# Performance work log

Measured on AMD Instinct MI355X. Metric: run time of the kernel, lower is better.

The kernel has to match this reference:

```python
import jax, jax.numpy as jnp
import numpy as np

B, N, D = 16, 512, 768
HEADS = 3
NEG_INF = -1e9


def _lin(k, o, i):
    s = 1.0 / np.sqrt(i)
    return jax.random.uniform(k, (o, i), jnp.float32, -s, s)


def setup_inputs() -> dict:
    key = jax.random.key(0)
    ks = jax.random.split(key, 20)
    adj = jax.random.uniform(ks[0], (B, N, N), jnp.float32)
    inputs = jax.random.normal(ks[1], (B, N, D), jnp.float32)
    # padding-style mask: last quarter of key positions masked (True = masked)
    score_mask = jnp.broadcast_to((jnp.arange(N) >= (3 * N) // 4)[None, None, None, :], (B, HEADS, N, N))
    Dh = 2 * D  # concat dim at layer 1
    return {
        'adj': adj,
        'inputs': inputs,
        'score_mask': score_mask,
        'W0_w': _lin(ks[2], D, D), 'W0_b': jnp.zeros((D,), jnp.float32),
        'W1_w': _lin(ks[3], D, Dh), 'W1_b': jnp.zeros((D,), jnp.float32),
        'conv_w': jax.random.normal(ks[4], (N, N, 3), jnp.float32) * (1.0 / np.sqrt(3 * N)),
        'conv_b': jnp.zeros((N,), jnp.float32),
        'linearc_w': _lin(ks[5], D, D - 2), 'linearc_b': jnp.zeros((D,), jnp.float32),
        'fc1_w': _lin(ks[6], D, D), 'fc2_w': _lin(ks[7], D, D),
        'attn_q_w': _lin(ks[8], Dh, Dh), 'attn_q_b': jnp.zeros((Dh,), jnp.float32),
        'attn_k_w': _lin(ks[9], Dh, Dh), 'attn_k_b': jnp.zeros((Dh,), jnp.float32),
    }


def _gcn_layer(adj, x, denom, Ww, Wb):
    Ax = jnp.einsum('bij,bjd->bid', adj, x)          # adj.bmm(x)
    AxW = (Ax @ Ww.T + Wb) / denom
    return jax.nn.relu(AxW) + (x @ Ww.T + Wb)


def reference(adj, inputs, score_mask, W0_w, W0_b, W1_w, W1_b, conv_w, conv_b,
              linearc_w, linearc_b, fc1_w, fc2_w, attn_q_w, attn_q_b, attn_k_w, attn_k_b):
    denom = adj.sum(2, keepdims=True) + 1.0
    out = _gcn_layer(adj, inputs, denom, W0_w, W0_b)            # [B,N,768]
    # Conv1d(n, n, 3): tokens as channels, features as length -> [B,N,766]
    conve = jax.lax.conv_general_dilated(out, conv_w, (1,), 'VALID',
                                         dimension_numbers=('NCH', 'OIH', 'NCH'))
    conve = jax.nn.relu(conve + conv_b[None, :, None])
    out = conve @ linearc_w.T + linearc_b                       # [B,N,768]

    x = jnp.concatenate([inputs, out], axis=-1)                 # [B,N,1536]
    Dh = x.shape[-1]
    d_k = Dh // HEADS
    q = (x @ attn_q_w.T + attn_q_b).reshape(B, N, HEADS, d_k).transpose(0, 2, 1, 3)
    k = (x @ attn_k_w.T + attn_k_b).reshape(B, N, HEADS, d_k).transpose(0, 2, 1, 3)
    scores = jnp.einsum('bhqd,bhkd->bhqk', q, k) / jnp.sqrt(jnp.float32(d_k))
    scores = jnp.where(score_mask, NEG_INF, scores)
    bmask = (~score_mask[:, :, :, 0:1]).astype(scores.dtype)    # [B,H,N,1]
    p_attn = jax.nn.softmax(scores, axis=-1) * bmask            # [B,H,N,N]

    sums = p_attn.sum(axis=(-2, -1))                            # [B,H]
    prob = jax.nn.softmax(sums, axis=0)                         # softmax over batch dim, as in source
    max_idx = jnp.argmax(prob, axis=1)                          # [B]
    adj2 = jnp.take_along_axis(p_attn, max_idx[:, None, None, None], axis=1)[:, 0]  # [B,N,N]

    # select(adj2, 2) * adj2 -- source mutates adj in place, so the RHS adj is binarized too
    flat = adj2.reshape(B, -1)
    thr = jax.lax.top_k(flat, 2)[0][:, 1]                       # 2nd-largest per batch
    bbin = (flat >= thr[:, None]).astype(adj2.dtype).reshape(B, N, N)
    M = bbin + jnp.swapaxes(bbin, -1, -2)
    eye = jnp.eye(N, dtype=adj2.dtype)
    M = M * (1.0 - eye) + eye                                   # fill_diagonal_(1)
    adj2 = M * bbin

    denom2 = adj2.sum(2, keepdims=True) + 1.0
    out = _gcn_layer(adj2, x, denom2, W1_w, W1_b)               # [B,N,768]
    out = jax.nn.relu(out @ fc1_w.T) @ fc2_w.T                  # fc (no biases)
    return out
```

## Files before the change

### kernel.cpp

```cpp
#include <hip/hip_runtime.h>
#include <math.h>


namespace {

constexpr long long O_DEN  = 0;
constexpr long long O_DEN2 = 8192;
constexpr long long O_SUMP = 16384;
constexpr long long O_THR  = 17920;
constexpr long long O_MIDX = 17936;
constexpr long long O_CNT  = 17952;
constexpr long long O_POS  = 17968;
constexpr long long O_T2P  = 18224;
constexpr long long O_NNZC = 19456;
constexpr long long O_NNZJ = 27648;
constexpr long long O_NNZV = 60416;
constexpr long long O_QKB  = 93184;

constexpr long long O_X    = 131072;
constexpr long long OZ     = 131072 + 12582912;
constexpr long long TOTAL_FLOATS = OZ + 17825792;

typedef short bf16x8 __attribute__((ext_vector_type(8)));
typedef float f32x4 __attribute__((ext_vector_type(4)));
typedef float f32x16 __attribute__((ext_vector_type(16)));

__global__ void sentinel_kernel(float* out) {
    if (threadIdx.x == 0 && blockIdx.x == 0) out[0] = 1.0e6f;
}

__device__ __forceinline__ unsigned short bf16rne(float f) {
    union { float x; unsigned u; } a; a.x = f;
    return (unsigned short)((a.u + 0x7FFFu + ((a.u >> 16) & 1u)) >> 16);
}

__device__ __forceinline__ void cvt_split(float f, unsigned short& h, unsigned short& l) {
    union { float x; unsigned u; } a; a.x = f;
    unsigned hb = (a.u + 0x7FFFu + ((a.u >> 16) & 1u)) & 0xFFFF0000u;
    h = (unsigned short)(hb >> 16);
    union { unsigned u; float x; } b; b.u = hb;
    float r = f - b.x;
    union { float x; unsigned u; } c; c.x = r;
    l = (unsigned short)((c.u + 0x7FFFu + ((c.u >> 16) & 1u)) >> 16);
}

__device__ __forceinline__ void gl_lds16(const unsigned short* g, unsigned short* l) {
    __builtin_amdgcn_global_load_lds(
        (const __attribute__((address_space(1))) unsigned int*)g,
        (__attribute__((address_space(3))) unsigned int*)l,
        16, 0, 0);
}

__global__ void convert_planes_kernel(const float* __restrict__ src, unsigned short* __restrict__ dst,
                                      long long loOff, long long n4) {
    long long idx = (long long)blockIdx.x * 256 + threadIdx.x;
    if (idx >= n4) return;
    float4 v = ((const float4*)src)[idx];
    unsigned short h0,h1,h2,h3,l0,l1,l2,l3;
    cvt_split(v.x,h0,l0); cvt_split(v.y,h1,l1); cvt_split(v.z,h2,l2); cvt_split(v.w,h3,l3);
    uint2 hp, lp;
    hp.x = (unsigned)h0 | ((unsigned)h1 << 16); hp.y = (unsigned)h2 | ((unsigned)h3 << 16);
    lp.x = (unsigned)l0 | ((unsigned)l1 << 16); lp.y = (unsigned)l2 | ((unsigned)l3 << 16);
    *(uint2*)&dst[idx * 4] = hp;
    *(uint2*)&dst[loOff + idx * 4] = lp;
}

__global__ void convert_bf16_kernel(const float* __restrict__ src, unsigned short* __restrict__ dst,
                                    long long n4) {
    long long idx = (long long)blockIdx.x * 256 + threadIdx.x;
    if (idx >= n4) return;
    float4 v = ((const float4*)src)[idx];
    ushort4 o;
    o.x = bf16rne(v.x); o.y = bf16rne(v.y); o.z = bf16rne(v.z); o.w = bf16rne(v.w);
    *(ushort4*)&dst[idx * 4] = o;
}

__global__ void transpose_bf16_kernel(const float* __restrict__ inp, unsigned short* __restrict__ dst) {
    __shared__ float T[64][65];
    const int z = blockIdx.z;
    const int i0 = blockIdx.x * 64, d0 = blockIdx.y * 64;
    const float* src = inp + (long long)z * 393216;
    unsigned short* dz = dst + (long long)z * 393216;
    const int cl = threadIdx.x & 63, rl = threadIdx.x >> 6;
    #pragma unroll 4
    for (int e = 0; e < 16; ++e) {
        int il = e * 4 + rl;
        T[il][cl] = src[(long long)(i0 + il) * 768 + d0 + cl];
    }
    __syncthreads();
    #pragma unroll 4
    for (int e = 0; e < 16; ++e) {
        int dl = e * 4 + rl;
        dz[(long long)(d0 + dl) * 512 + i0 + cl] = bf16rne(T[cl][dl]);
    }
}

__global__ void pad_lw_kernel(const float* __restrict__ Lw, unsigned short* __restrict__ Lp) {
    int idx = blockIdx.x * 256 + threadIdx.x;
    int n = idx / 768, k = idx - n * 768;
    float v = (k < 766) ? Lw[n * 766 + k] : 0.f;
    unsigned short h, l; cvt_split(v, h, l);
    Lp[idx] = h; Lp[589824 + idx] = l;
}

__global__ void convert_qkw_kernel(const float* __restrict__ Qw, const float* __restrict__ Kw,
                                   unsigned short* __restrict__ dst) {
    long long idx = (long long)blockIdx.x * 256 + threadIdx.x;
    if (idx >= 1179648) return;
    long long e = idx * 4;
    int h = (int)(e / 1572864);
    int rem = (int)(e - (long long)h * 1572864);
    int row = rem / 1536, k = rem - row * 1536;
    const float* src = (row < 512) ? (Qw + ((long long)(h * 512 + row) * 1536 + k))
                                   : (Kw + ((long long)(h * 512 + row - 512) * 1536 + k));
    float4 v = *(const float4*)src;
    unsigned short h0,h1,h2,h3,l0,l1,l2,l3;
    cvt_split(v.x,h0,l0); cvt_split(v.y,h1,l1); cvt_split(v.z,h2,l2); cvt_split(v.w,h3,l3);
    uint2 hp, lp;
    hp.x = (unsigned)h0 | ((unsigned)h1 << 16); hp.y = (unsigned)h2 | ((unsigned)h3 << 16);
    lp.x = (unsigned)l0 | ((unsigned)l1 << 16); lp.y = (unsigned)l2 | ((unsigned)l3 << 16);
    *(uint2*)&dst[e] = hp;
    *(uint2*)&dst[4718592 + e] = lp;
}

__global__ void qkb_kernel(const float* __restrict__ Qb, const float* __restrict__ Kb,
                           float* __restrict__ qkb) {
    int i = blockIdx.x * 256 + threadIdx.x;
    if (i >= 3072) return;
    int h = i >> 10, r = i & 1023;
    qkb[i] = (r < 512) ? Qb[h * 512 + r] : Kb[h * 512 + r - 512];
}

template<int TAG, int BMODE, int CMODE, int ONEPASS>
__global__ __launch_bounds__(256, ONEPASS ? 3 : 2)
void gemm_mfma_kernel(const unsigned short* __restrict__ Au, const void* __restrict__ Bv,
                      void* __restrict__ Cv, const float* __restrict__ bias,
                      int M, int N, int K, int lda, int ldb, int ldc,
                      long long sA, long long sB, long long sC,
                      float divd, int relu, long long aLo,
                      long long bLo, long long cLo, int Nreal)
{
    __shared__ __align__(16) unsigned short AhS[2][128][32];
    __shared__ __align__(16) unsigned short BhS[2][128][32];
    __shared__ __align__(16) unsigned short AlS[ONEPASS ? 1 : 2][128][32];
    __shared__ __align__(16) unsigned short BlS[ONEPASS ? 1 : 2][128][32];

    const int gx = gridDim.x, gy = gridDim.y;
    const int nwg = gx * gy * gridDim.z;
    const int lin = blockIdx.x + gx * (blockIdx.y + gy * blockIdx.z);
    const int q8 = nwg >> 3, r8 = nwg & 7;
    const int xcd = lin & 7, sidx = lin >> 3;
    const int nl = (xcd < r8) ? xcd * (q8 + 1) + sidx : r8 * (q8 + 1) + (xcd - r8) * q8 + sidx;
    const int bx = nl % gx;
    const int t1 = nl / gx;
    const int by = t1 % gy;
    const int z  = t1 / gy;

    const int tid = threadIdx.x;
    const int m0 = by * 128, n0 = bx * 128;
    const int lane = tid & 63, wave = tid >> 6;
    const int wm = (wave & 1) * 64, wn = (wave >> 1) * 64;
    const int lk = lane >> 5, lm = lane & 31;
    const int sxor = (lm >> 1) & 3;

    const unsigned short* A = Au + z * sA;
    const float* Bf = (const float*)Bv + z * sB;
    const unsigned short* Bu = (const unsigned short*)Bv + z * sB;
    float* Cf = (float*)Cv + z * sC;
    unsigned short* Cu = (unsigned short*)Cv + z * sC;

    f32x16 acc[2][2];
    #pragma unroll
    for (int i = 0; i < 2; ++i)
        #pragma unroll
        for (int j = 0; j < 2; ++j)
            #pragma unroll
            for (int r = 0; r < 16; ++r) acc[i][j][r] = 0.f;

    auto stage = [&](int kk, int b) {
        #pragma unroll
        for (int v = 0; v < 2; ++v) {
            const int j0 = v * 256 + (wave << 6);
            const int row0 = j0 >> 2;
            const int j = j0 + lane;
            const int row = j >> 2, c = j & 3;
            const int kch = c ^ ((row >> 1) & 3);
            const long long aoff = (long long)(m0 + row) * lda + kk + kch * 8;
            gl_lds16(A + aoff, &AhS[b][row0][0]);
            if constexpr (!ONEPASS) gl_lds16(A + aLo + aoff, &AlS[b][row0][0]);
            if constexpr (BMODE == 3) {
                const long long boff = (long long)(n0 + row) * ldb + kk + kch * 8;
                gl_lds16(Bu + boff, &BhS[b][row0][0]);
                if constexpr (!ONEPASS) gl_lds16(Bu + bLo + boff, &BlS[b][row0][0]);
            }
        }
        if constexpr (BMODE == 2) {
            #pragma unroll
            for (int v = 0; v < 2; ++v) {
                const int j = v * 256 + tid;
                const int n = j >> 2, c = j & 3;
                const int kch = c ^ ((n >> 1) & 3);
                const int k8 = kk + kch * 8;
                unsigned short hh[8], ll[8];
                #pragma unroll
                for (int e = 0; e < 8; ++e) {
                    const int kg = k8 + e;
                    const int ii = kg / 3, k3 = kg - ii * 3;
                    cvt_split(Bf[(long long)ii * 768 + (n0 + n) + k3], hh[e], ll[e]);
                }
                uint4 hp, lp;
                hp.x = (unsigned)hh[0] | ((unsigned)hh[1] << 16);
                hp.y = (unsigned)hh[2] | ((unsigned)hh[3] << 16);
                hp.z = (unsigned)hh[4] | ((unsigned)hh[5] << 16);
                hp.w = (unsigned)hh[6] | ((unsigned)hh[7] << 16);
                lp.x = (unsigned)ll[0] | ((unsigned)ll[1] << 16);
                lp.y = (unsigned)ll[2] | ((unsigned)ll[3] << 16);
                lp.z = (unsigned)ll[4] | ((unsigned)ll[5] << 16);
                lp.w = (unsigned)ll[6] | ((unsigned)ll[7] << 16);
                *(uint4*)&BhS[b][n][c * 8] = hp;
                *(uint4*)&BlS[b][n][c * 8] = lp;
            }
        }
    };

    auto compute = [&](int b) {
        #pragma unroll
        for (int ks = 0; ks < 2; ++ks) {
            const int kc = ks * 2 + lk;
            const int sl = (kc ^ sxor) * 8;
            bf16x8 ah[2], bh[2];
            #pragma unroll
            for (int i = 0; i < 2; ++i) ah[i] = *(const bf16x8*)&AhS[b][wm + i * 32 + lm][sl];
            #pragma unroll
            for (int j = 0; j < 2; ++j) bh[j] = *(const bf16x8*)&BhS[b][wn + j * 32 + lm][sl];
            if constexpr (ONEPASS) {
                #pragma unroll
                for (int i = 0; i < 2; ++i)
                    #pragma unroll
                    for (int j = 0; j < 2; ++j)
                        acc[i][j] = __builtin_amdgcn_mfma_f32_32x32x16_bf16(ah[i], bh[j], acc[i][j], 0, 0, 0);
            } else {
                bf16x8 al[2], bl[2];
                #pragma unroll
                for (int i = 0; i < 2; ++i) al[i] = *(const bf16x8*)&AlS[b][wm + i * 32 + lm][sl];
                #pragma unroll
                for (int j = 0; j < 2; ++j) bl[j] = *(const bf16x8*)&BlS[b][wn + j * 32 + lm][sl];
                #pragma unroll
                for (int i = 0; i < 2; ++i)
                    #pragma unroll
                    for (int j = 0; j < 2; ++j) {
                        acc[i][j] = __builtin_amdgcn_mfma_f32_32x32x16_bf16(ah[i], bh[j], acc[i][j], 0, 0, 0);
                        acc[i][j] = __builtin_amdgcn_mfma_f32_32x32x16_bf16(ah[i], bl[j], acc[i][j], 0, 0, 0);
                        acc[i][j] = __builtin_amdgcn_mfma_f32_32x32x16_bf16(al[i], bh[j], acc[i][j], 0, 0, 0);
                    }
            }
        }
    };

    const int nt = K >> 5;
    stage(0, 0);
    for (int t = 0; t < nt; ++t) {
        if constexpr (BMODE == 2) {
            asm volatile("s_waitcnt vmcnt(0) lgkmcnt(0)" ::: "memory");
        } else {
            asm volatile("s_waitcnt vmcnt(0)" ::: "memory");
        }
        __builtin_amdgcn_sched_barrier(0);
        __builtin_amdgcn_s_barrier();
        __builtin_amdgcn_sched_barrier(0);
        if (t + 1 < nt) stage((t + 1) << 5, (t + 1) & 1);
        __builtin_amdgcn_s_setprio(1);
        compute(t & 1);
        __builtin_amdgcn_s_setprio(0);
    }
    #pragma unroll
    for (int i = 0; i < 2; ++i) {
        #pragma unroll
        for (int j = 0; j < 2; ++j) {
            #pragma unroll
            for (int reg = 0; reg < 16; ++reg) {
                const int m = m0 + wm + i * 32 + (reg & 3) + 8 * (reg >> 2) + 4 * lk;
                const int n = n0 + wn + j * 32 + lm;
                float v = acc[i][j][reg];
                if (divd != 1.f) v = v / divd;
                if (bias) v += bias[BMODE == 2 ? m : n];
                if (relu) v = fmaxf(v, 0.f);
                if (n >= Nreal) v = 0.f;
                if constexpr (CMODE == 1) {
                    unsigned short h, l; cvt_split(v, h, l);
                    Cu[(long long)m * ldc + n] = h;
                    Cu[cLo + (long long)m * ldc + n] = l;
                } else {
                    Cf[(long long)m * ldc + n] = v;
                }
            }
        }
    }
}

__global__ void rowsum_kernel(const float* __restrict__ A, float* __restrict__ out, int ncols) {
    const float* row = A + (long long)blockIdx.x * ncols;
    float s = 0.f;
    for (int j = threadIdx.x; j < ncols; j += 256) s += row[j];
    __shared__ float red[256];
    red[threadIdx.x] = s;
    __syncthreads();
    for (int st = 128; st > 0; st >>= 1) {
        if (threadIdx.x < st) red[threadIdx.x] += red[threadIdx.x + st];
        __syncthreads();
    }
    if (threadIdx.x == 0) out[blockIdx.x] = red[0] + 1.0f;
}

__global__ void gcn_epilogue_kernel(const float* __restrict__ axw, const float* __restrict__ xw,
                                    const float* __restrict__ bias, const float* __restrict__ denom,
                                    float* __restrict__ out)
{
    long long idx = (long long)blockIdx.x * 256 + threadIdx.x;
    int m = (int)(idx / 768);
    int d = (int)(idx - (long long)m * 768);
    float bb = bias[d];
    float v = (axw[idx] + bb) / denom[m];
    out[idx] = fmaxf(v, 0.f) + xw[idx] + bb;
}

__global__ void copy_concat_kernel(const float* __restrict__ inp, unsigned short* __restrict__ xcat)
{
    long long idx = (long long)blockIdx.x * 256 + threadIdx.x;
    int m = (int)(idx / 768);
    int d = (int)(idx - (long long)m * 768);
    unsigned short h, l; cvt_split(inp[idx], h, l);
    xcat[(long long)m * 1536 + d] = h;
    xcat[12582912LL + (long long)m * 1536 + d] = l;
}

__global__ void softmax_kernel(float* __restrict__ P)
{
    float* row = P + (long long)blockIdx.x * 384;
    const int t = threadIdx.x;
    float v0 = row[t], v1 = row[t + 128], v2 = row[t + 256];
    float m = fmaxf(v0, fmaxf(v1, v2));
    #pragma unroll
    for (int off = 32; off > 0; off >>= 1) m = fmaxf(m, __shfl_down(m, off));
    __shared__ float redm[2];
    if ((t & 63) == 0) redm[t >> 6] = m;
    __syncthreads();
    m = fmaxf(redm[0], redm[1]);
    float e0 = expf(v0 - m), e1 = expf(v1 - m), e2 = expf(v2 - m);
    float s = e0 + e1 + e2;
    #pragma unroll
    for (int off = 32; off > 0; off >>= 1) s += __shfl_down(s, off);
    __shared__ float reds[2];
    if ((t & 63) == 0) reds[t >> 6] = s;
    __syncthreads();
    s = reds[0] + reds[1];
    row[t] = e0 / s;
    row[t + 128] = e1 / s;
    row[t + 256] = e2 / s;
}

__global__ void sums1_kernel(const float* __restrict__ P, double* __restrict__ sump)
{
    int blk = blockIdx.x;
    int bh = blk >> 4, ch = blk & 15;
    const float* p = P + (long long)bh * 196608 + ch * 12288;
    double s = 0.0;
    for (int i = threadIdx.x; i < 12288; i += 256) s += (double)p[i];
    __shared__ double red[256];
    red[threadIdx.x] = s;
    __syncthreads();
    for (int st = 128; st > 0; st >>= 1) {
        if (threadIdx.x < st) red[threadIdx.x] += red[threadIdx.x + st];
        __syncthreads();
    }
    if (threadIdx.x == 0) sump[blk] = red[0];
}

__global__ void decide2_kernel(const double* __restrict__ sump, int* __restrict__ maxidx)
{
    __shared__ double s48[48];
    int t = threadIdx.x;
    if (t < 48) {
        double s = 0.0;
        for (int i = 0; i < 16; ++i) s += sump[t * 16 + i];
        s48[t] = s;
    }
    __syncthreads();
    if (t == 0) {
        float s[16][3], prob[16][3];
        for (int b = 0; b < 16; ++b)
            for (int h = 0; h < 3; ++h) s[b][h] = (float)s48[b * 3 + h];
        for (int h = 0; h < 3; ++h) {
            float m = -1e30f;
            for (int b = 0; b < 16; ++b) m = fmaxf(m, s[b][h]);
            float e[16]; float Z = 0.f;
            for (int b = 0; b < 16; ++b) { e[b] = expf(s[b][h] - m); Z += e[b]; }
            for (int b = 0; b < 16; ++b) prob[b][h] = e[b] / Z;
        }
        for (int b = 0; b < 16; ++b) {
            int best = 0; float bv = prob[b][0];
            for (int h = 1; h < 3; ++h) if (prob[b][h] > bv) { bv = prob[b][h]; best = h; }
            maxidx[b] = best;
        }
    }
}

__global__ void top2a_kernel(const float* __restrict__ P, const int* __restrict__ maxidx,
                             float2* __restrict__ t2p)
{
    int blk = blockIdx.x;
    int b = blk >> 5, ch = blk & 31;
    const float* p = P + ((long long)b * 3 + maxidx[b]) * 196608 + ch * 6144;
    float m1 = -1e30f, m2 = -1e30f;
    for (int i = threadIdx.x; i < 6144; i += 256) {
        float v = p[i];
        if (v > m1) { m2 = m1; m1 = v; }
        else if (v > m2) { m2 = v; }
    }
    __shared__ float r1[256], r2[256];
    r1[threadIdx.x] = m1; r2[threadIdx.x] = m2;
    __syncthreads();
    if (threadIdx.x == 0) {
        float M1 = -1e30f, M2 = -1e30f;
        for (int i = 0; i < 256; ++i) {
            float a = r1[i], c = r2[i];
            if (a > M1) { M2 = M1; M1 = a; } else if (a > M2) { M2 = a; }
            if (c > M1) { M2 = M1; M1 = c; } else if (c > M2) { M2 = c; }
        }
        t2p[blk] = make_float2(M1, M2);
    }
}

__global__ void top2b_kernel(const float2* __restrict__ t2p, float* __restrict__ thr)
{
    int b = blockIdx.x;
    if (threadIdx.x != 0) return;
    float M1 = -1e30f, M2 = -1e30f;
    for (int i = 0; i < 32; ++i) {
        float2 v = t2p[b * 32 + i];
        if (v.x > M1) { M2 = M1; M1 = v.x; } else if (v.x > M2) { M2 = v.x; }
        if (v.y > M1) { M2 = M1; M1 = v.y; } else if (v.y > M2) { M2 = v.y; }
    }
    thr[b] = M2;
}

__global__ void init_nnz_kernel(int* __restrict__ cntb, int* __restrict__ nnzc,
                                float* __restrict__ den2)
{
    int idx = blockIdx.x * 256 + threadIdx.x;
    if (idx < 16) cntb[idx] = 0;
    if (idx < 8192) { nnzc[idx] = 0; den2[idx] = 1.f; }
}

__global__ void scan_thr_kernel(const float* __restrict__ P, const int* __restrict__ maxidx,
                                const float* __restrict__ thr, int* __restrict__ cntb,
                                int* __restrict__ pos)
{
    int blk = blockIdx.x;
    int b = blk / 12, ch = blk % 12;
    const float* p = P + ((long long)b * 3 + maxidx[b]) * 196608;
    float t = thr[b];
    int base = ch * 16384;
    for (int l = 0; l < 64; ++l) {
        int idx = base + threadIdx.x + l * 256;
        if (p[idx] >= t) {
            int q = atomicAdd(&cntb[b], 1);
            if (q < 16) {
                int i = idx / 384, j = idx - i * 384;
                pos[b * 16 + q] = (i << 16) | j;
            }
        }
    }
}

__global__ void build_nnz_kernel(const int* __restrict__ cntb, const int* __restrict__ pos,
                                 int* __restrict__ nnzc, int* __restrict__ jn,
                                 float* __restrict__ jv, float* __restrict__ den2)
{
    int b = threadIdx.x;
    if (b >= 16 || blockIdx.x != 0) return;
    int c = cntb[b]; if (c > 16) c = 16;
    for (int e = 0; e < c; ++e) {
        int pk = pos[b * 16 + e];
        int i = pk >> 16, j = pk & 0xFFFF;
        float val;
        if (i == j) val = 1.f;
        else {
            int rev = (j << 16) | i;
            int found = 0;
            for (int e2 = 0; e2 < c; ++e2) if (pos[b * 16 + e2] == rev) found = 1;
            val = 1.f + (float)found;
        }
        int r = b * 512 + i;
        int slot = nnzc[r];
        if (slot < 4) { jn[r * 4 + slot] = b * 512 + j; jv[r * 4 + slot] = val; }
        nnzc[r] = slot + 1;
        den2[r] += val;
    }
}

__global__ void gcn1_epilogue_kernel(const float* __restrict__ XW1, const float* __restrict__ b1,
                                     const float* __restrict__ den2, const int* __restrict__ cnt,
                                     const int* __restrict__ jn, const float* __restrict__ jv,
                                     unsigned short* __restrict__ outp)
{
    int m = blockIdx.x;
    int c = cnt[m]; if (c > 4) c = 4;
    float d2 = den2[m];
    int js[4]; float vs[4];
    for (int s = 0; s < c; ++s) { js[s] = jn[m * 4 + s]; vs[s] = jv[m * 4 + s]; }
    const float* xrow = XW1 + (long long)m * 768;
    #pragma unroll
    for (int l = 0; l < 3; ++l) {
        int d = threadIdx.x + l * 256;
        float ax = 0.f;
        for (int s = 0; s < c; ++s) ax += vs[s] * XW1[(long long)js[s] * 768 + d];
        float bb = b1[d];
        float v = fmaxf((ax + bb) / d2, 0.f) + xrow[d] + bb;
        unsigned short h, lo; cvt_split(v, h, lo);
        outp[(long long)m * 768 + d] = h;
        outp[6291456LL + (long long)m * 768 + d] = lo;
    }
}

}

extern "C" void kernel_launch(void* const* d_in, const int* in_sizes, int n_in,
                              void* d_out, int out_size, void* d_ws, size_t ws_size,
                              hipStream_t stream) {
    const float* adj = (const float*)d_in[0];
    const float* inp = (const float*)d_in[1];
    const float* W0w = (const float*)d_in[3];
    const float* W0b = (const float*)d_in[4];
    const float* W1w = (const float*)d_in[5];
    const float* W1b = (const float*)d_in[6];
    const float* Cw  = (const float*)d_in[7];
    const float* Cbi = (const float*)d_in[8];
    const float* Lw  = (const float*)d_in[9];
    const float* Lb  = (const float*)d_in[10];
    const float* F1  = (const float*)d_in[11];
    const float* F2  = (const float*)d_in[12];
    const float* Qw  = (const float*)d_in[13];
    const float* Qb  = (const float*)d_in[14];
    const float* Kw  = (const float*)d_in[15];
    const float* Kbi = (const float*)d_in[16];
    float* out = (float*)d_out;

    if (ws_size < (size_t)TOTAL_FLOATS * sizeof(float)) {
        sentinel_kernel<<<dim3(1), dim3(64), 0, stream>>>(out);
        return;
    }

    float* W = (float*)d_ws;
    float*   DEN   = W + O_DEN;
    float*   DEN2  = W + O_DEN2;
    double*  SUMP  = (double*)(W + O_SUMP);
    float*   THR   = W + O_THR;
    int*     MIDX  = (int*)(W + O_MIDX);
    int*     CNT   = (int*)(W + O_CNT);
    int*     POS   = (int*)(W + O_POS);
    float2*  T2P   = (float2*)(W + O_T2P);
    int*     NNZC  = (int*)(W + O_NNZC);
    int*     NNZJ  = (int*)(W + O_NNZJ);
    float*   NNZV  = W + O_NNZV;
    float*   QKB   = W + O_QKB;

    unsigned short* INPP  = (unsigned short*)(W + O_X);
    float*          OUT0  = W + O_X;
    unsigned short* XCATp = (unsigned short*)(W + O_X);
    unsigned short* F1P   = (unsigned short*)(W + O_X);
    unsigned short* F2P   = (unsigned short*)(W + O_X + 589824);

    unsigned short* AXp    = (unsigned short*)(W + OZ);
    float*          AXW0f  = W + OZ + 6291456;
    float*          XW0f   = W + O_X + 6291456;
    unsigned short* W0P    = (unsigned short*)(W + OZ + 12582912);
    unsigned short* ADJB   = (unsigned short*)(W + OZ + 13172736);
    unsigned short* CONVEp = (unsigned short*)(W + OZ);
    unsigned short* CwP    = (unsigned short*)(W + OZ + 6291456);
    unsigned short* LWPp   = (unsigned short*)(W + OZ + 7077888);
    unsigned short* QKp    = (unsigned short*)(W + OZ);
    float*          P      = W + OZ + 8388608;
    float*          XW1f   = W + OZ;
    unsigned short* OUTL1p = (unsigned short*)(W + OZ + 6291456);
    unsigned short* H1p    = (unsigned short*)(W + OZ);

    unsigned short* INPTB  = (unsigned short*)out;
    unsigned short* QKwP   = (unsigned short*)out;
    unsigned short* W1P    = (unsigned short*)(out + 4718592);

    const float divs = sqrtf(512.0f);
    const int BIGN = 1 << 30;

    convert_planes_kernel<<<dim3(6144), dim3(256), 0, stream>>>(inp, INPP, 6291456, 1572864);
    convert_planes_kernel<<<dim3(576), dim3(256), 0, stream>>>(W0w, W0P, 589824, 147456);
    convert_bf16_kernel<<<dim3(4096), dim3(256), 0, stream>>>(adj, ADJB, 1048576);
    transpose_bf16_kernel<<<dim3(8, 12, 16), dim3(256), 0, stream>>>(inp, INPTB);
    qkb_kernel<<<dim3(12), dim3(256), 0, stream>>>(Qb, Kbi, QKB);
    rowsum_kernel<<<dim3(8192), dim3(256), 0, stream>>>(adj, DEN, 512);
    gemm_mfma_kernel<0, 3, 1, 1><<<dim3(6, 4, 16), dim3(256), 0, stream>>>(
        ADJB, INPTB, AXp, nullptr, 512, 768, 512, 512, 512, 768,
        262144LL, 393216LL, 393216LL, 1.f, 0, 0, 0, 6291456LL, BIGN);
    gemm_mfma_kernel<1, 3, 0, 0><<<dim3(6, 64, 2), dim3(256), 0, stream>>>(
        INPP, W0P, XW0f, nullptr, 8192, 768, 768, 768, 768, 768,
        25165824LL, 0, 12582912LL, 1.f, 0, 6291456LL, 589824LL, 0, BIGN);
    gcn_epilogue_kernel<<<dim3(24576), dim3(256), 0, stream>>>(AXW0f, XW0f, W0b, DEN, OUT0);

    convert_planes_kernel<<<dim3(768), dim3(256), 0, stream>>>(Cw, CwP, 786432, 196608);
    pad_lw_kernel<<<dim3(2304), dim3(256), 0, stream>>>(Lw, LWPp);
    convert_qkw_kernel<<<dim3(4608), dim3(256), 0, stream>>>(Qw, Kw, QKwP);
    convert_planes_kernel<<<dim3(1152), dim3(256), 0, stream>>>(W1w, W1P, 1179648, 294912);

    gemm_mfma_kernel<2, 2, 1, 0><<<dim3(6, 4, 16), dim3(256), 0, stream>>>(
        CwP, OUT0, CONVEp, Cbi, 512, 768, 1536, 1536, 0, 768,
        0, 393216LL, 393216LL, 1.f, 1, 786432LL, 0, 6291456LL, 766);
    gemm_mfma_kernel<3, 3, 1, 0><<<dim3(6, 64, 1), dim3(256), 0, stream>>>(
        CONVEp, LWPp, (void*)(XCATp + 768), Lb, 8192, 768, 768, 768, 768, 1536,
        0, 0, 0, 1.f, 0, 6291456LL, 589824LL, 12582912LL, BIGN);
    copy_concat_kernel<<<dim3(24576), dim3(256), 0, stream>>>(inp, XCATp);

    for (int h = 0; h < 3; ++h) {
        gemm_mfma_kernel<4, 3, 1, 0><<<dim3(8, 64, 1), dim3(256), 0, stream>>>(
            XCATp, QKwP + (long long)h * 1572864, QKp, QKB + h * 1024,
            8192, 1024, 1536, 1536, 1536, 1024,
            0, 0, 0, 1.f, 0, 12582912LL, 4718592LL, 8388608LL, BIGN);
        gemm_mfma_kernel<5, 3, 0, 0><<<dim3(3, 4, 16), dim3(256), 0, stream>>>(
            QKp, QKp + 512, P + (long long)h * 196608, nullptr,
            512, 384, 512, 1024, 1024, 384,
            524288LL, 524288LL, 589824LL, divs, 0, 8388608LL, 8388608LL, 0, BIGN);
    }

    softmax_kernel<<<dim3(24576), dim3(128), 0, stream>>>(P);
    sums1_kernel<<<dim3(768), dim3(256), 0, stream>>>(P, SUMP);
    decide2_kernel<<<dim3(1), dim3(64), 0, stream>>>(SUMP, MIDX);
    top2a_kernel<<<dim3(512), dim3(256), 0, stream>>>(P, MIDX, T2P);
    top2b_kernel<<<dim3(16), dim3(64), 0, stream>>>(T2P, THR);
    init_nnz_kernel<<<dim3(32), dim3(256), 0, stream>>>(CNT, NNZC, DEN2);
    scan_thr_kernel<<<dim3(192), dim3(256), 0, stream>>>(P, MIDX, THR, CNT, POS);
    build_nnz_kernel<<<dim3(1), dim3(64), 0, stream>>>(CNT, POS, NNZC, NNZJ, NNZV, DEN2);

    gemm_mfma_kernel<6, 3, 0, 0><<<dim3(6, 64, 1), dim3(256), 0, stream>>>(
        XCATp, W1P, XW1f, nullptr, 8192, 768, 1536, 1536, 1536, 768,
        0, 0, 0, 1.f, 0, 12582912LL, 1179648LL, 0, BIGN);
    convert_planes_kernel<<<dim3(576), dim3(256), 0, stream>>>(F1, F1P, 589824, 147456);
    convert_planes_kernel<<<dim3(576), dim3(256), 0, stream>>>(F2, F2P, 589824, 147456);
    gcn1_epilogue_kernel<<<dim3(8192), dim3(256), 0, stream>>>(XW1f, W1b, DEN2, NNZC, NNZJ, NNZV, OUTL1p);
    gemm_mfma_kernel<7, 3, 1, 0><<<dim3(6, 64, 1), dim3(256), 0, stream>>>(
        OUTL1p, F1P, H1p, nullptr, 8192, 768, 768, 768, 768, 768,
        0, 0, 0, 1.f, 1, 6291456LL, 589824LL, 6291456LL, BIGN);
    gemm_mfma_kernel<8, 3, 0, 0><<<dim3(6, 64, 1), dim3(256), 0, stream>>>(
        H1p, F2P, out, nullptr, 8192, 768, 768, 768, 768, 768,
        0, 0, 0, 1.f, 0, 6291456LL, 589824LL, 0, BIGN);
}
```

Before: 1.119 ms.

## Enlarge GEMM tile to 256x128 with 8 waves and two-stage prefetch pipeline

The MFMA GEMM block grows from 256 to 512 threads, and the M tile doubles to 256 rows, so each B tile loaded into LDS is reused across twice as many rows. All launches are updated to halve the grid in y. For the BMODE==3 path, loads are now issued two stages ahead with partial vmcnt waits and a trailing barrier, so memory latency overlaps more of the compute. The larger LDS footprint and 512-thread blocks lower the number of resident blocks and leave fewer blocks for the small batched GEMMs.

New measurement: 1.150 ms. 1.03x slower.

```diff
diff --git a/kernel.cpp b/kernel.cpp
--- a/kernel.cpp
+++ b/kernel.cpp
@@ -132,7 +132,7 @@
 }
 
 template<int TAG, int BMODE, int CMODE, int ONEPASS>
-__global__ __launch_bounds__(256, ONEPASS ? 3 : 2)
+__global__ __launch_bounds__(512, 2)
 void gemm_mfma_kernel(const unsigned short* __restrict__ Au, const void* __restrict__ Bv,
                       void* __restrict__ Cv, const float* __restrict__ bias,
                       int M, int N, int K, int lda, int ldb, int ldc,
@@ -140,9 +140,9 @@
                       float divd, int relu, long long aLo,
                       long long bLo, long long cLo, int Nreal)
 {
-    __shared__ __align__(16) unsigned short AhS[2][128][32];
+    __shared__ __align__(16) unsigned short AhS[2][256][32];
     __shared__ __align__(16) unsigned short BhS[2][128][32];
-    __shared__ __align__(16) unsigned short AlS[ONEPASS ? 1 : 2][128][32];
+    __shared__ __align__(16) unsigned short AlS[ONEPASS ? 1 : 2][256][32];
     __shared__ __align__(16) unsigned short BlS[ONEPASS ? 1 : 2][128][32];
 
     const int gx = gridDim.x, gy = gridDim.y;
@@ -157,9 +157,9 @@
     const int z  = t1 / gy;
 
     const int tid = threadIdx.x;
-    const int m0 = by * 128, n0 = bx * 128;
+    const int m0 = by * 256, n0 = bx * 128;
     const int lane = tid & 63, wave = tid >> 6;
-    const int wm = (wave & 1) * 64, wn = (wave >> 1) * 64;
+    const int wm = (wave & 3) * 64, wn = (wave >> 2) * 64;
     const int lk = lane >> 5, lm = lane & 31;
     const int sxor = (lm >> 1) & 3;
 
@@ -179,8 +179,8 @@
 
     auto stage = [&](int kk, int b) {
         #pragma unroll
-        for (int v = 0; v < 2; ++v) {
-            const int j0 = v * 256 + (wave << 6);
+        for (int l = 0; l < 2; ++l) {
+            const int j0 = (wave << 7) + (l << 6);
             const int row0 = j0 >> 2;
             const int j = j0 + lane;
             const int row = j >> 2, c = j & 3;
@@ -188,38 +188,38 @@
             const long long aoff = (long long)(m0 + row) * lda + kk + kch * 8;
             gl_lds16(A + aoff, &AhS[b][row0][0]);
             if constexpr (!ONEPASS) gl_lds16(A + aLo + aoff, &AlS[b][row0][0]);
-            if constexpr (BMODE == 3) {
-                const long long boff = (long long)(n0 + row) * ldb + kk + kch * 8;
-                gl_lds16(Bu + boff, &BhS[b][row0][0]);
-                if constexpr (!ONEPASS) gl_lds16(Bu + bLo + boff, &BlS[b][row0][0]);
+        }
+        if constexpr (BMODE == 3) {
+            const int j0 = wave << 6;
+            const int row0 = j0 >> 2;
+            const int j = j0 + lane;
+            const int row = j >> 2, c = j & 3;
+            const int kch = c ^ ((row >> 1) & 3);
+            const long long boff = (long long)(n0 + row) * ldb + kk + kch * 8;
+            gl_lds16(Bu + boff, &BhS[b][row0][0]);
+            if constexpr (!ONEPASS) gl_lds16(Bu + bLo + boff, &BlS[b][row0][0]);
+        } else {
+            const int n = tid >> 2, c = tid & 3;
+            const int kch = c ^ ((n >> 1) & 3);
+            const int k8 = kk + kch * 8;
+            unsigned short hh[8], ll[8];
+            #pragma unroll
+            for (int e = 0; e < 8; ++e) {
+                const int kg = k8 + e;
+                const int ii = kg / 3, k3 = kg - ii * 3;
+                cvt_split(Bf[(long long)ii * 768 + (n0 + n) + k3], hh[e], ll[e]);
             }
-        }
-        if constexpr (BMODE == 2) {
-            #pragma unroll
-            for (int v = 0; v < 2; ++v) {
-                const int j = v * 256 + tid;
-                const int n = j >> 2, c = j & 3;
-                const int kch = c ^ ((n >> 1) & 3);
-                const int k8 = kk + kch * 8;
-                unsigned short hh[8], ll[8];
-                #pragma unroll
-                for (int e = 0; e < 8; ++e) {
-                    const int kg = k8 + e;
-                    const int ii = kg / 3, k3 = kg - ii * 3;
-                    cvt_split(Bf[(long long)ii * 768 + (n0 + n) + k3], hh[e], ll[e]);
-                }
-                uint4 hp, lp;
-                hp.x = (unsigned)hh[0] | ((unsigned)hh[1] << 16);
-                hp.y = (unsigned)hh[2] | ((unsigned)hh[3] << 16);
-                hp.z = (unsigned)hh[4] | ((unsigned)hh[5] << 16);
-                hp.w = (unsigned)hh[6] | ((unsigned)hh[7] << 16);
-                lp.x = (unsigned)ll[0] | ((unsigned)ll[1] << 16);
-                lp.y = (unsigned)ll[2] | ((unsigned)ll[3] << 16);
-                lp.z = (unsigned)ll[4] | ((unsigned)ll[5] << 16);
-                lp.w = (unsigned)ll[6] | ((unsigned)ll[7] << 16);
-                *(uint4*)&BhS[b][n][c * 8] = hp;
-                *(uint4*)&BlS[b][n][c * 8] = lp;
-            }
+            uint4 hp, lp;
+            hp.x = (unsigned)hh[0] | ((unsigned)hh[1] << 16);
+            hp.y = (unsigned)hh[2] | ((unsigned)hh[3] << 16);
+            hp.z = (unsigned)hh[4] | ((unsigned)hh[5] << 16);
+            hp.w = (unsigned)hh[6] | ((unsigned)hh[7] << 16);
+            lp.x = (unsigned)ll[0] | ((unsigned)ll[1] << 16);
+            lp.y = (unsigned)ll[2] | ((unsigned)ll[3] << 16);
+            lp.z = (unsigned)ll[4] | ((unsigned)ll[5] << 16);
+            lp.w = (unsigned)ll[6] | ((unsigned)ll[7] << 16);
+            *(uint4*)&BhS[b][n][c * 8] = hp;
+            *(uint4*)&BlS[b][n][c * 8] = lp;
         }
     };
 
@@ -258,20 +258,38 @@
     };
 
     const int nt = K >> 5;
-    stage(0, 0);
-    for (int t = 0; t < nt; ++t) {
-        if constexpr (BMODE == 2) {
+    if constexpr (BMODE == 3) {
+        stage(0, 0);
+        if (nt > 1) stage(32, 1);
+        for (int t = 0; t < nt; ++t) {
+            if (t + 1 < nt) {
+                if constexpr (ONEPASS) { asm volatile("s_waitcnt vmcnt(3)" ::: "memory"); }
+                else                   { asm volatile("s_waitcnt vmcnt(6)" ::: "memory"); }
+            } else {
+                asm volatile("s_waitcnt vmcnt(0)" ::: "memory");
+            }
+            __builtin_amdgcn_sched_barrier(0);
+            __builtin_amdgcn_s_barrier();
+            __builtin_amdgcn_sched_barrier(0);
+            __builtin_amdgcn_s_setprio(1);
+            compute(t & 1);
+            __builtin_amdgcn_s_setprio(0);
+            __builtin_amdgcn_sched_barrier(0);
+            __builtin_amdgcn_s_barrier();
+            if (t + 2 < nt) stage((t + 2) << 5, t & 1);
+        }
+    } else {
+        stage(0, 0);
+        for (int t = 0; t < nt; ++t) {
             asm volatile("s_waitcnt vmcnt(0) lgkmcnt(0)" ::: "memory");
-        } else {
-            asm volatile("s_waitcnt vmcnt(0)" ::: "memory");
-        }
-        __builtin_amdgcn_sched_barrier(0);
-        __builtin_amdgcn_s_barrier();
-        __builtin_amdgcn_sched_barrier(0);
-        if (t + 1 < nt) stage((t + 1) << 5, (t + 1) & 1);
-        __builtin_amdgcn_s_setprio(1);
-        compute(t & 1);
-        __builtin_amdgcn_s_setprio(0);
+            __builtin_amdgcn_sched_barrier(0);
+            __builtin_amdgcn_s_barrier();
+            __builtin_amdgcn_sched_barrier(0);
+            if (t + 1 < nt) stage((t + 1) << 5, (t + 1) & 1);
+            __builtin_amdgcn_s_setprio(1);
+            compute(t & 1);
+            __builtin_amdgcn_s_setprio(0);
+        }
     }
     #pragma unroll
     for (int i = 0; i < 2; ++i) {
@@ -598,10 +616,10 @@
     transpose_bf16_kernel<<<dim3(8, 12, 16), dim3(256), 0, stream>>>(inp, INPTB);
     qkb_kernel<<<dim3(12), dim3(256), 0, stream>>>(Qb, Kbi, QKB);
     rowsum_kernel<<<dim3(8192), dim3(256), 0, stream>>>(adj, DEN, 512);
-    gemm_mfma_kernel<0, 3, 1, 1><<<dim3(6, 4, 16), dim3(256), 0, stream>>>(
+    gemm_mfma_kernel<0, 3, 1, 1><<<dim3(6, 2, 16), dim3(512), 0, stream>>>(
         ADJB, INPTB, AXp, nullptr, 512, 768, 512, 512, 512, 768,
         262144LL, 393216LL, 393216LL, 1.f, 0, 0, 0, 6291456LL, BIGN);
-    gemm_mfma_kernel<1, 3, 0, 0><<<dim3(6, 64, 2), dim3(256), 0, stream>>>(
+    gemm_mfma_kernel<1, 3, 0, 0><<<dim3(6, 32, 2), dim3(512), 0, stream>>>(
         INPP, W0P, XW0f, nullptr, 8192, 768, 768, 768, 768, 768,
         25165824LL, 0, 12582912LL, 1.f, 0, 6291456LL, 589824LL, 0, BIGN);
     gcn_epilogue_kernel<<<dim3(24576), dim3(256), 0, stream>>>(AXW0f, XW0f, W0b, DEN, OUT0);
@@ -611,20 +629,20 @@
     convert_qkw_kernel<<<dim3(4608), dim3(256), 0, stream>>>(Qw, Kw, QKwP);
     convert_planes_kernel<<<dim3(1152), dim3(256), 0, stream>>>(W1w, W1P, 1179648, 294912);
 
-    gemm_mfma_kernel<2, 2, 1, 0><<<dim3(6, 4, 16), dim3(256), 0, stream>>>(
+    gemm_mfma_kernel<2, 2, 1, 0><<<dim3(6, 2, 16), dim3(512), 0, stream>>>(
         CwP, OUT0, CONVEp, Cbi, 512, 768, 1536, 1536, 0, 768,
         0, 393216LL, 393216LL, 1.f, 1, 786432LL, 0, 6291456LL, 766);
-    gemm_mfma_kernel<3, 3, 1, 0><<<dim3(6, 64, 1), dim3(256), 0, stream>>>(
+    gemm_mfma_kernel<3, 3, 1, 0><<<dim3(6, 32, 1), dim3(512), 0, stream>>>(
         CONVEp, LWPp, (void*)(XCATp + 768), Lb, 8192, 768, 768, 768, 768, 1536,
         0, 0, 0, 1.f, 0, 6291456LL, 589824LL, 12582912LL, BIGN);
     copy_concat_kernel<<<dim3(24576), dim3(256), 0, stream>>>(inp, XCATp);
 
     for (int h = 0; h < 3; ++h) {
-        gemm_mfma_kernel<4, 3, 1, 0><<<dim3(8, 64, 1), dim3(256), 0, stream>>>(
+        gemm_mfma_kernel<4, 3, 1, 0><<<dim3(8, 32, 1), dim3(512), 0, stream>>>(
             XCATp, QKwP + (long long)h * 1572864, QKp, QKB + h * 1024,
             8192, 1024, 1536, 1536, 1536, 1024,
             0, 0, 0, 1.f, 0, 12582912LL, 4718592LL, 8388608LL, BIGN);
-        gemm_mfma_kernel<5, 3, 0, 0><<<dim3(3, 4, 16), dim3(256), 0, stream>>>(
+        gemm_mfma_kernel<5, 3, 0, 0><<<dim3(3, 2, 16), dim3(512), 0, stream>>>(
             QKp, QKp + 512, P + (long long)h * 196608, nullptr,
             512, 384, 512, 1024, 1024, 384,
             524288LL, 524288LL, 589824LL, divs, 0, 8388608LL, 8388608LL, 0, BIGN);
@@ -639,16 +657,16 @@
     scan_thr_kernel<<<dim3(192), dim3(256), 0, stream>>>(P, MIDX, THR, CNT, POS);
     build_nnz_kernel<<<dim3(1), dim3(64), 0, stream>>>(CNT, POS, NNZC, NNZJ, NNZV, DEN2);
 
-    gemm_mfma_kernel<6, 3, 0, 0><<<dim3(6, 64, 1), dim3(256), 0, stream>>>(
+    gemm_mfma_kernel<6, 3, 0, 0><<<dim3(6, 32, 1), dim3(512), 0, stream>>>(
         XCATp, W1P, XW1f, nullptr, 8192, 768, 1536, 1536, 1536, 768,
         0, 0, 0, 1.f, 0, 12582912LL, 1179648LL, 0, BIGN);
     convert_planes_kernel<<<dim3(576), dim3(256), 0, stream>>>(F1, F1P, 589824, 147456);
     convert_planes_kernel<<<dim3(576), dim3(256), 0, stream>>>(F2, F2P, 589824, 147456);
     gcn1_epilogue_kernel<<<dim3(8192), dim3(256), 0, stream>>>(XW1f, W1b, DEN2, NNZC, NNZJ, NNZV, OUTL1p);
-    gemm_mfma_kernel<7, 3, 1, 0><<<dim3(6, 64, 1), dim3(256), 0, stream>>>(
+    gemm_mfma_kernel<7, 3, 1, 0><<<dim3(6, 32, 1), dim3(512), 0, stream>>>(
         OUTL1p, F1P, H1p, nullptr, 8192, 768, 768, 768, 768, 768,
         0, 0, 0, 1.f, 1, 6291456LL, 589824LL, 6291456LL, BIGN);
-    gemm_mfma_kernel<8, 3, 0, 0><<<dim3(6, 64, 1), dim3(256), 0, stream>>>(
+    gemm_mfma_kernel<8, 3, 0, 0><<<dim3(6, 32, 1), dim3(512), 0, stream>>>(
         H1p, F2P, out, nullptr, 8192, 768, 768, 768, 768, 768,
         0, 0, 0, 1.f, 0, 6291456LL, 589824LL, 0, BIGN);
 }
```
